# Kernel optimization log

Hardware: AMD Instinct MI355X
Metric: run time of the kernel (lower is better)

The kernel has to match this reference:

```python
import jax, jax.numpy as jnp
import numpy as np

# dims: G groups, A authors/group, P posts/author, DIN token-pooled feat, DEMB sentence-BERT dim
G, A, P, DIN, DEMB, HP, HA = 16, 64, 32, 768, 384, 256, 128


def setup_inputs() -> dict:
    key = jax.random.key(0)
    ks = jax.random.split(key, 8)
    s = lambda k, shape, scale: (jax.random.normal(k, shape, jnp.float32) * scale)
    return {
        "x": jax.random.normal(ks[0], (G, A, P, DIN), jnp.float32),
        "w_embed": s(ks[1], (DIN, DEMB), 0.02),   # BERT pooled-projection stand-in
        "b_embed": jnp.zeros((DEMB,), jnp.float32),
        "k_post": s(ks[2], (DEMB, 4 * HP), 0.05),  # Keras LSTM kernel, gates [i|f|c|o]
        "r_post": s(ks[3], (HP, 4 * HP), 0.05),    # recurrent kernel
        "b_post": jnp.zeros((4 * HP,), jnp.float32),
        "k_auth": s(ks[4], (HP, 4 * HA), 0.05),
        "r_auth": s(ks[5], (HA, 4 * HA), 0.05),
        "b_auth": jnp.zeros((4 * HA,), jnp.float32),
    }


def _lstm(x, Wk, Wr, b):
    """Keras-style LSTM, returns final hidden state. x: [B,T,D] -> [B,H]."""
    B = x.shape[0]
    H = Wr.shape[0]
    # precompute input projections for all timesteps in one GEMM: [T,B,4H]
    z = jnp.einsum('btd,dh->tbh', x, Wk) + b

    def step(carry, zt):
        h, c = carry
        g = zt + h @ Wr
        i, f, gg, o = jnp.split(g, 4, axis=-1)  # Keras gate order i,f,c,o
        c = jax.nn.sigmoid(f) * c + jax.nn.sigmoid(i) * jnp.tanh(gg)
        h = jax.nn.sigmoid(o) * jnp.tanh(c)
        return (h, c), None

    h0 = jnp.zeros((B, H), x.dtype)
    (h, _), _ = jax.lax.scan(step, (h0, h0), z)
    return h


def reference(x, w_embed, b_embed, k_post, r_post, b_post, k_auth, r_auth, b_auth):
    g, a, p, _ = x.shape
    # sentence embedding per post (BERT stand-in): [G,A,P,DEMB]
    e = jnp.einsum('gapd,de->gape', x, w_embed) + b_embed
    # LSTM over posts, batched across all (group, author) pairs: [G,A,HP]
    h_post = _lstm(e.reshape(g * a, p, e.shape[-1]), k_post, r_post, b_post)
    h_post = h_post.reshape(g, a, -1)
    # LSTM over authors: [G,HA]
    return _lstm(h_post, k_auth, r_auth, b_auth)
```

## Files before the change

### kernel.cpp

```cpp
#include <hip/hip_runtime.h>
#include <cstdint>
#include <cstddef>

#define G_    16
#define A_    64
#define P_    32
#define DIN_  768
#define DEMB_ 384
#define HP_   256
#define HA_   128
#define GA_   1024
#define N1_   1024
#define N2_   512
#define TCH   16

typedef float    f32x4   __attribute__((ext_vector_type(4)));
typedef _Float16 half8_t __attribute__((ext_vector_type(8)));
typedef _Float16 half4_t __attribute__((ext_vector_type(4)));

__device__ __forceinline__ float sigmoidf_(float x) { return 1.0f / (1.0f + __expf(-x)); }
__device__ __forceinline__ float tanhf_(float x) { return 2.0f / (1.0f + __expf(-2.0f * x)) - 1.0f; }
__device__ __forceinline__ _Float16 us2h(unsigned short u) { _Float16 h; __builtin_memcpy(&h, &u, 2); return h; }
__device__ __forceinline__ unsigned short h2us(_Float16 h) { unsigned short u; __builtin_memcpy(&u, &h, 2); return u; }


__global__ __launch_bounds__(256) void k_wk(const float* __restrict__ w_embed,
                                            const float* __restrict__ k_post,
                                            float* __restrict__ Bmat) {
    int j  = blockIdx.x * 256 + threadIdx.x;
    int k0 = blockIdx.y * 4;
    float acc0 = 0.f, acc1 = 0.f, acc2 = 0.f, acc3 = 0.f;
    for (int d = 0; d < DEMB_; ++d) {
        float kp = k_post[(size_t)d * N1_ + j];
        acc0 += w_embed[(size_t)(k0 + 0) * DEMB_ + d] * kp;
        acc1 += w_embed[(size_t)(k0 + 1) * DEMB_ + d] * kp;
        acc2 += w_embed[(size_t)(k0 + 2) * DEMB_ + d] * kp;
        acc3 += w_embed[(size_t)(k0 + 3) * DEMB_ + d] * kp;
    }
    Bmat[(size_t)(k0 + 0) * N1_ + j] = acc0;
    Bmat[(size_t)(k0 + 1) * N1_ + j] = acc1;
    Bmat[(size_t)(k0 + 2) * N1_ + j] = acc2;
    Bmat[(size_t)(k0 + 3) * N1_ + j] = acc3;
}

__global__ __launch_bounds__(256) void k_bias_p(const float* __restrict__ b_embed,
                                                const float* __restrict__ k_post,
                                                const float* __restrict__ b_post,
                                                float* __restrict__ biasZp) {
    int p = blockIdx.x * 256 + threadIdx.x;
    int n = (p >> 6) * 16 + (p & 15) + 256 * ((p >> 4) & 3);
    float acc = b_post[n];
    for (int d = 0; d < DEMB_; ++d)
        acc += b_embed[d] * k_post[(size_t)d * N1_ + n];
    biasZp[p] = acc;
}

__global__ __launch_bounds__(256) void k_t16(const float* __restrict__ Bmat,
                                             _Float16* __restrict__ Bt16) {
    __shared__ float tile[64][65];
    const int tid = threadIdx.x;
    const int p0 = blockIdx.x * 64;
    const int k0 = blockIdx.y * 64;
    const int jgrp = p0 >> 6;
#pragma unroll
    for (int i = 0; i < 16; ++i) {
        int idx = i * 256 + tid;
        int pp = idx & 63, kk = idx >> 6;
        int n = jgrp * 16 + (pp & 15) + 256 * ((pp >> 4) & 3);
        tile[pp][kk] = Bmat[(size_t)(k0 + kk) * N1_ + n];
    }
    __syncthreads();
    const int pp = tid >> 2;
    const int kq = (tid & 3) * 16;
    _Float16 buf[16];
#pragma unroll
    for (int i = 0; i < 16; ++i) buf[i] = (_Float16)tile[pp][kq + i];
    _Float16* dst = &Bt16[(size_t)(p0 + pp) * DIN_ + k0 + kq];
    *(half8_t*)dst       = *(half8_t*)&buf[0];
    *(half8_t*)(dst + 8) = *(half8_t*)&buf[8];
}

__global__ __launch_bounds__(256) void k_bfrag(const float* __restrict__ r_post,
                                               _Float16* __restrict__ Bfrag) {
    int idx = blockIdx.x * 256 + threadIdx.x;
    int pt = idx >> 9;
    int kt = (idx >> 6) & 7;
    int l  = idx & 63;
    int p = pt * 16 + (l & 15);
    int n = (p >> 6) * 16 + (p & 15) + 256 * ((p >> 4) & 3);
    int kb = kt * 32 + (l >> 4) * 8;
    _Float16 buf[8];
#pragma unroll
    for (int s = 0; s < 8; ++s) buf[s] = (_Float16)r_post[(size_t)(kb + s) * N1_ + n];
    *(half8_t*)&Bfrag[(size_t)idx * 8] = *(half8_t*)buf;
}

#define ZBM 128
#define ZBN 256
#define ZBK 32
#define ZPAD 40

struct ZgLDS {
    union {
        struct { _Float16 As[ZBM][ZPAD]; _Float16 Bs[ZBN][ZPAD]; } S;
        _Float16 Hs[64][264];
    } u;
};
struct RecLDS {
    _Float16 wlds[16 * 8 * 64 * 8];
    _Float16 hbuf[2][4096];
};

__device__ __forceinline__ void zgemm_core(ZgLDS* L, int bid, int tid,
                                           const float* __restrict__ x,
                                           const _Float16* __restrict__ Bt16,
                                           const float* __restrict__ biasZp,
                                           _Float16* __restrict__ Zq, int tbase) {
    const int wg = (bid & 7) * 64 + (bid >> 3);
    const int bm = (wg & 127) * ZBM;
    const int bn = (wg >> 7) * ZBN;

    const int arow = tid >> 3, akq = (tid & 7) * 4;
    const int brow = tid >> 2, bkq = (tid & 3) * 8;
    const int lane = tid & 63, w = tid >> 6;
    const int wm = (w >> 2) * 32, wn = (w & 3) * 64;
    const int frc = lane & 15, frk = (lane >> 4) * 8;

    const int crow = bm + arow;
    const size_t xrow = (size_t)(crow >> 4) * P_ + tbase + (crow & 15);
    const float*    aptr = &x[xrow * DIN_ + akq];
    const _Float16* bptr = &Bt16[(size_t)(bn + brow) * DIN_ + bkq];

    f32x4 acc[2][4];
#pragma unroll
    for (int i = 0; i < 2; ++i)
#pragma unroll
        for (int j = 0; j < 4; ++j) acc[i][j] = (f32x4)0.0f;

    float4 a0 = *(const float4*)aptr;
    uint4  b0 = *(const uint4*)bptr;

    const int NK = DIN_ / ZBK;
    for (int kt = 0; kt < NK; ++kt) {
        const int kn = (kt + 1 < NK) ? (kt + 1) * ZBK : kt * ZBK;
        float4 na0 = *(const float4*)(aptr + kn);
        uint4  nb0 = *(const uint4*)(bptr + kn);

        half4_t ahv;
        ahv[0] = (_Float16)a0.x; ahv[1] = (_Float16)a0.y;
        ahv[2] = (_Float16)a0.z; ahv[3] = (_Float16)a0.w;

        __syncthreads();
        *(half4_t*)&L->u.S.As[arow][akq] = ahv;
        *(uint4*)&L->u.S.Bs[brow][bkq]   = b0;
        __syncthreads();

        half8_t bf[4];
#pragma unroll
        for (int fn = 0; fn < 4; ++fn)
            bf[fn] = *(const half8_t*)&L->u.S.Bs[wn + fn * 16 + frc][frk];
#pragma unroll
        for (int fm = 0; fm < 2; ++fm) {
            half8_t aH = *(const half8_t*)&L->u.S.As[wm + fm * 16 + frc][frk];
#pragma unroll
            for (int fn = 0; fn < 4; ++fn)
                acc[fm][fn] = __builtin_amdgcn_mfma_f32_16x16x32_f16(aH, bf[fn], acc[fm][fn], 0, 0, 0);
        }
        a0 = na0; b0 = nb0;
    }

    float bzv[4];
#pragma unroll
    for (int fn = 0; fn < 4; ++fn) bzv[fn] = biasZp[bn + wn + fn * 16 + frc];

#pragma unroll
    for (int half_ = 0; half_ < 2; ++half_) {
        __syncthreads();
        if ((w >> 3) == half_) {
#pragma unroll
            for (int fm = 0; fm < 2; ++fm)
#pragma unroll
                for (int fn = 0; fn < 4; ++fn)
#pragma unroll
                    for (int r = 0; r < 4; ++r) {
                        int rl = ((w >> 2) & 1) * 32 + fm * 16 + (lane >> 4) * 4 + r;
                        int cl = wn + fn * 16 + frc;
                        int clp = ((cl >> 6) * 16 + (cl & 15)) * 4 + ((cl >> 4) & 3);
                        L->u.Hs[rl][clp] = (_Float16)(acc[fm][fn][r] + bzv[fn]);
                    }
        }
        __syncthreads();
        const int brb = (bm + half_ * 64) >> 4;
        const int rg  = brb >> 4;
        const int l4r = (brb & 15) >> 2;
        {
            int tloc = tid >> 6, hcl = tid & 63;
            _Float16 buf[16];
#pragma unroll
            for (int rr = 0; rr < 4; ++rr) {
                half4_t h4 = *(const half4_t*)&L->u.Hs[tloc + 16 * rr][hcl * 4];
                buf[rr * 4 + 0] = h4[0]; buf[rr * 4 + 1] = h4[1];
                buf[rr * 4 + 2] = h4[2]; buf[rr * 4 + 3] = h4[3];
            }
            int wvg  = (bn >> 6) + (hcl >> 4);
            int tid2 = wvg * 64 + l4r * 16 + (hcl & 15);
            _Float16* dst = &Zq[((size_t)(tloc * 64 + rg) * 1024 + tid2) * 16];
            *(uint4*)dst       = *(const uint4*)&buf[0];
            *(uint4*)(dst + 8) = *(const uint4*)&buf[8];
        }
    }
}

__device__ __forceinline__ void rec_core(RecLDS* L, int blk, int tid,
                                         const _Float16* __restrict__ Zq,
                                         const _Float16* __restrict__ Bfrag,
                                         float* __restrict__ csave,
                                         unsigned short* __restrict__ hsave,
                                         float* __restrict__ hF32, int tbase) {
    const int lane = tid & 63, wv = tid >> 6;
    const int hl = lane & 15, l4 = lane >> 4;
    const int r0 = blk * 16;
    const int hc = wv * 16 + hl;

    half8_t wreg[16];
#pragma unroll
    for (int q = 0; q < 2; ++q)
#pragma unroll
        for (int kt = 0; kt < 8; ++kt)
            wreg[q * 8 + kt] = *(const half8_t*)&Bfrag[(((size_t)(4 * wv + q) * 8 + kt) * 64 + lane) * 8];
#pragma unroll
    for (int kt = 0; kt < 8; ++kt)
        *(half8_t*)&L->wlds[((wv * 8 + kt) * 64 + lane) * 8] =
            *(const half8_t*)&Bfrag[(((size_t)(4 * wv + 2) * 8 + kt) * 64 + lane) * 8];
    const _Float16* w3base = &Bfrag[((size_t)(4 * wv + 3) * 8 * 64 + lane) * 8];

    float cst[4];
    if (tbase == 0) {
#pragma unroll
        for (int i = 0; i < 4; ++i) cst[i] = 0.f;
    } else {
        f32x4 cv = *(const f32x4*)&csave[((size_t)blk * 1024 + tid) * 4];
#pragma unroll
        for (int i = 0; i < 4; ++i) cst[i] = cv[i];
#pragma unroll
        for (int rr = 0; rr < 4; ++rr) {
            int row = l4 * 4 + rr;
            int lidx = (((hc >> 5) * 64) + (((hc & 31) >> 3) * 16 + row)) * 8 + (hc & 7);
            L->hbuf[0][lidx] = us2h(hsave[((size_t)(r0 + row)) * HP_ + hc]);
        }
    }
    __syncthreads();

    const _Float16* zp0 = &Zq[((size_t)blk * 1024 + tid) * 16];
    half8_t z01N = *(const half8_t*)zp0;
    half8_t z23N = *(const half8_t*)(zp0 + 8);

    for (int tt = 0; tt < TCH; ++tt) {
        const int t = tbase + tt;
        const int cur = t & 1, nxt = cur ^ 1;

        half8_t z01 = z01N, z23 = z23N;
        if (tt + 1 < TCH) {
            const _Float16* zpn = zp0 + (size_t)(tt + 1) * 1048576;
            z01N = *(const half8_t*)zpn;
            z23N = *(const half8_t*)(zpn + 8);
        }

        f32x4 acc[4];
#pragma unroll
        for (int i = 0; i < 4; ++i) acc[i] = (f32x4)0.0f;

        if (t > 0) {
#pragma unroll
            for (int kt = 0; kt < 8; ++kt) {
                half8_t ah = *(const half8_t*)&L->hbuf[cur][(kt * 64 + lane) * 8];
                half8_t b2 = *(const half8_t*)&L->wlds[((wv * 8 + kt) * 64 + lane) * 8];
                half8_t w3 = *(const half8_t*)&w3base[(size_t)kt * 512];
                acc[0] = __builtin_amdgcn_mfma_f32_16x16x32_f16(ah, wreg[kt],     acc[0], 0, 0, 0);
                acc[1] = __builtin_amdgcn_mfma_f32_16x16x32_f16(ah, wreg[8 + kt], acc[1], 0, 0, 0);
                acc[2] = __builtin_amdgcn_mfma_f32_16x16x32_f16(ah, b2,           acc[2], 0, 0, 0);
                acc[3] = __builtin_amdgcn_mfma_f32_16x16x32_f16(ah, w3,           acc[3], 0, 0, 0);
            }
        }

        const bool last = (t == P_ - 1);
        const bool save = (tbase == 0) && (tt == TCH - 1);
#pragma unroll
        for (int rr = 0; rr < 4; ++rr) {
            const half8_t zsrc = (rr < 2) ? z01 : z23;
            const int o = (rr & 1) * 4;
            float gi = acc[0][rr] + (float)zsrc[o + 0];
            float gf = acc[1][rr] + (float)zsrc[o + 1];
            float gg = acc[2][rr] + (float)zsrc[o + 2];
            float go = acc[3][rr] + (float)zsrc[o + 3];
            float cn = sigmoidf_(gf) * cst[rr] + sigmoidf_(gi) * tanhf_(gg);
            cst[rr] = cn;
            float hv = sigmoidf_(go) * tanhf_(cn);
            int row = l4 * 4 + rr;
            int lidx = (((hc >> 5) * 64) + (((hc & 31) >> 3) * 16 + row)) * 8 + (hc & 7);
            _Float16 hh = (_Float16)hv;
            L->hbuf[nxt][lidx] = hh;
            if (save) hsave[((size_t)(r0 + row)) * HP_ + hc] = h2us(hh);
            if (last) hF32[(size_t)(r0 + row) * HP_ + hc] = hv;
        }
        __syncthreads();
    }

    if (tbase == 0) {
        f32x4 cv;
#pragma unroll
        for (int i = 0; i < 4; ++i) cv[i] = cst[i];
        *(f32x4*)&csave[((size_t)blk * 1024 + tid) * 4] = cv;
    }
}

__global__ __launch_bounds__(1024, 4) void k_zgemm(const float* __restrict__ x,
                                                   const _Float16* __restrict__ Bt16,
                                                   const float* __restrict__ biasZp,
                                                   _Float16* __restrict__ Zq, int tbase) {
    __shared__ __align__(16) ZgLDS L;
    zgemm_core(&L, blockIdx.x, threadIdx.x, x, Bt16, biasZp, Zq, tbase);
}

__global__ __launch_bounds__(1024, 4) void k_rec(const _Float16* __restrict__ Zq,
                                                 const _Float16* __restrict__ Bfrag,
                                                 float* __restrict__ csave,
                                                 unsigned short* __restrict__ hsave,
                                                 float* __restrict__ hF32, int tbase) {
    __shared__ __align__(16) RecLDS L;
    rec_core(&L, blockIdx.x, threadIdx.x, Zq, Bfrag, csave, hsave, hF32, tbase);
}

__global__ __launch_bounds__(1024, 4) void k_fuse(const float* __restrict__ x,
                                                  const _Float16* __restrict__ Bt16,
                                                  const float* __restrict__ biasZp,
                                                  const _Float16* __restrict__ Zq0,
                                                  _Float16* __restrict__ Zq1,
                                                  const _Float16* __restrict__ Bfrag,
                                                  float* __restrict__ csave,
                                                  unsigned short* __restrict__ hsave,
                                                  float* __restrict__ hF32) {
    __shared__ __align__(16) union { RecLDS r; ZgLDS z; } L;
    if (blockIdx.x < 64)
        rec_core(&L.r, blockIdx.x, threadIdx.x, Zq0, Bfrag, csave, hsave, hF32, 0);
    else
        zgemm_core(&L.z, blockIdx.x - 64, threadIdx.x, x, Bt16, biasZp, Zq1, TCH);
}

__global__ __launch_bounds__(256) void k_zauth(const float* __restrict__ h,
                                               const float* __restrict__ k_auth,
                                               const float* __restrict__ b_auth,
                                               float* __restrict__ z_auth) {
    const int j = blockIdx.x * 256 + threadIdx.x;
    const int r0 = blockIdx.y * 4;
    float acc0 = b_auth[j], acc1 = acc0, acc2 = acc0, acc3 = acc0;
    for (int k = 0; k < HP_; ++k) {
        const float kp = k_auth[(size_t)k * N2_ + j];
        acc0 += h[(size_t)(r0 + 0) * HP_ + k] * kp;
        acc1 += h[(size_t)(r0 + 1) * HP_ + k] * kp;
        acc2 += h[(size_t)(r0 + 2) * HP_ + k] * kp;
        acc3 += h[(size_t)(r0 + 3) * HP_ + k] * kp;
    }
#pragma unroll
    for (int r = 0; r < 4; ++r) {
        const int b = r0 + r;
        const int g = b >> 6, a = b & 63;
        const float v = (r == 0) ? acc0 : (r == 1) ? acc1 : (r == 2) ? acc2 : acc3;
        z_auth[((size_t)a * G_ + g) * N2_ + j] = v;
    }
}

__global__ __launch_bounds__(1024) void k_author(const float* __restrict__ z_auth,
                                                 const float* __restrict__ r_auth,
                                                 float* __restrict__ out) {
    const int g = blockIdx.x;
    const int tid = threadIdx.x;
    const int j = tid & 511;
    const int kh = tid >> 9;

    __shared__ float hs[HA_];
    __shared__ float parts[2][512];

    float rc[64];
#pragma unroll
    for (int kk = 0; kk < 64; ++kk)
        rc[kk] = r_auth[(size_t)(kh * 64 + kk) * N2_ + j];

    float cj = 0.f;
    if (tid < HA_) hs[tid] = 0.f;
    __syncthreads();

    for (int a = 0; a < A_; ++a) {
        float acc = (kh == 0) ? z_auth[((size_t)a * G_ + g) * N2_ + j] : 0.f;
#pragma unroll
        for (int kk = 0; kk < 64; ++kk)
            acc += hs[kh * 64 + kk] * rc[kk];
        parts[kh][j] = acc;
        __syncthreads();
        if (tid < HA_) {
            float gi = parts[0][tid]       + parts[1][tid];
            float gf = parts[0][tid + 128] + parts[1][tid + 128];
            float gg = parts[0][tid + 256] + parts[1][tid + 256];
            float go = parts[0][tid + 384] + parts[1][tid + 384];
            cj = sigmoidf_(gf) * cj + sigmoidf_(gi) * tanhf_(gg);
            hs[tid] = sigmoidf_(go) * tanhf_(cj);
        }
        __syncthreads();
    }
    if (tid < HA_) out[(size_t)g * HA_ + tid] = hs[tid];
}

extern "C" void kernel_launch(void* const* d_in, const int* in_sizes, int n_in,
                              void* d_out, int out_size, void* d_ws, size_t ws_size,
                              hipStream_t stream) {
    const float* x       = (const float*)d_in[0];
    const float* w_embed = (const float*)d_in[1];
    const float* b_embed = (const float*)d_in[2];
    const float* k_post  = (const float*)d_in[3];
    const float* r_post  = (const float*)d_in[4];
    const float* b_post  = (const float*)d_in[5];
    const float* k_auth  = (const float*)d_in[6];
    const float* r_auth  = (const float*)d_in[7];
    const float* b_auth  = (const float*)d_in[8];
    float* out = (float*)d_out;

    char* wsb = (char*)d_ws;
    _Float16*       Zq0    = (_Float16*)(wsb);
    float*          Bmat   = (float*)(wsb + (32ull << 20));
    _Float16*       Bt16   = (_Float16*)(wsb + (36ull << 20));
    _Float16*       Bfrag  = (_Float16*)(wsb + (38ull << 20));
    float*          biasZp = (float*)(wsb + (38ull << 20) + (512ull << 10));
    float*          csave  = (float*)(wsb + (39ull << 20));
    unsigned short* hsave  = (unsigned short*)(wsb + (40ull << 20));
    float*          hF32   = (float*)(wsb + (41ull << 20));
    float*          z_auth = (float*)(wsb + (42ull << 20));
    _Float16*       Zq1    = (_Float16*)(wsb + (44ull << 20));

    const bool overlap = (ws_size >= (77ull << 20));

    k_wk    <<<dim3(N1_ / 256, DIN_ / 4), 256, 0, stream>>>(w_embed, k_post, Bmat);
    k_bias_p<<<dim3(N1_ / 256), 256, 0, stream>>>(b_embed, k_post, b_post, biasZp);
    k_t16   <<<dim3(16, 12), 256, 0, stream>>>(Bmat, Bt16);
    k_bfrag <<<dim3(128), 256, 0, stream>>>(r_post, Bfrag);

    k_zgemm<<<dim3(512), 1024, 0, stream>>>(x, Bt16, biasZp, Zq0, 0);

    if (overlap) {
        k_fuse<<<dim3(576), 1024, 0, stream>>>(x, Bt16, biasZp, Zq0, Zq1,
                                               Bfrag, csave, hsave, hF32);
        k_rec <<<dim3(64), 1024, 0, stream>>>(Zq1, Bfrag, csave, hsave, hF32, TCH);
    } else {
        k_rec  <<<dim3(64), 1024, 0, stream>>>(Zq0, Bfrag, csave, hsave, hF32, 0);
        k_zgemm<<<dim3(512), 1024, 0, stream>>>(x, Bt16, biasZp, Zq0, TCH);
        k_rec  <<<dim3(64), 1024, 0, stream>>>(Zq0, Bfrag, csave, hsave, hF32, TCH);
    }

    k_zauth <<<dim3(N2_ / 256, GA_ / 4), 256, 0, stream>>>(hF32, k_auth, b_auth, z_auth);
    k_author<<<dim3(G_), 1024, 0, stream>>>(z_auth, r_auth, out);
}
```

Baseline: 337.1 us.

## Pipeline input-projection GEMM and post LSTM per timestep via global flags

Replaces the two-chunk scheme (GEMM half, then fused rec+GEMM, then rec) with one persistent kernel. GEMM blocks each produce one timestep tile and bump a per-timestep atomic counter, and the 64 recurrence blocks spin on those counters before consuming each step. This removes the intermediate c/h save/restore and extra launches, and lets the recurrence start as soon as step 0 is ready. It relies on the recurrence blocks being co-resident with the GEMM blocks and on forward progress of the spin-waits; if scheduling orders blocks badly, this could deadlock or stall. The prefetch of the next step's Z is also removed.

```diff
diff --git a/kernel.cpp b/kernel.cpp
--- a/kernel.cpp
+++ b/kernel.cpp
@@ -111,14 +111,16 @@
     _Float16 hbuf[2][4096];
 };
 
-__device__ __forceinline__ void zgemm_core(ZgLDS* L, int bid, int tid,
-                                           const float* __restrict__ x,
-                                           const _Float16* __restrict__ Bt16,
-                                           const float* __restrict__ biasZp,
-                                           _Float16* __restrict__ Zq, int tbase) {
-    const int wg = (bid & 7) * 64 + (bid >> 3);
-    const int bm = (wg & 127) * ZBM;
-    const int bn = (wg >> 7) * ZBN;
+__device__ __forceinline__ void zg_t_core(ZgLDS* L, int b2, int tid,
+                                          const float* __restrict__ x,
+                                          const _Float16* __restrict__ Bt16,
+                                          const float* __restrict__ biasZp,
+                                          _Float16* __restrict__ Zq,
+                                          int* __restrict__ flags) {
+    const int t  = b2 >> 5;
+    const int tl = b2 & 31;
+    const int bm = (tl >> 2) * ZBM;
+    const int bn = (tl & 3) * ZBN;
 
     const int arow = tid >> 3, akq = (tid & 7) * 4;
     const int brow = tid >> 2, bkq = (tid & 3) * 8;
@@ -127,8 +129,7 @@
     const int frc = lane & 15, frk = (lane >> 4) * 8;
 
     const int crow = bm + arow;
-    const size_t xrow = (size_t)(crow >> 4) * P_ + tbase + (crow & 15);
-    const float*    aptr = &x[xrow * DIN_ + akq];
+    const float*    aptr = &x[((size_t)crow * P_ + t) * DIN_ + akq];
     const _Float16* bptr = &Bt16[(size_t)(bn + brow) * DIN_ + bkq];
 
     f32x4 acc[2][4];
@@ -190,33 +191,38 @@
                     }
         }
         __syncthreads();
-        const int brb = (bm + half_ * 64) >> 4;
-        const int rg  = brb >> 4;
-        const int l4r = (brb & 15) >> 2;
+        const int B0 = bm + half_ * 64;
         {
-            int tloc = tid >> 6, hcl = tid & 63;
+            int g4 = tid >> 6, hcl = tid & 63;
             _Float16 buf[16];
 #pragma unroll
             for (int rr = 0; rr < 4; ++rr) {
-                half4_t h4 = *(const half4_t*)&L->u.Hs[tloc + 16 * rr][hcl * 4];
+                half4_t h4 = *(const half4_t*)&L->u.Hs[g4 * 4 + rr][hcl * 4];
                 buf[rr * 4 + 0] = h4[0]; buf[rr * 4 + 1] = h4[1];
                 buf[rr * 4 + 2] = h4[2]; buf[rr * 4 + 3] = h4[3];
             }
+            int rg   = (B0 >> 4) + (g4 >> 2);
+            int l4r  = g4 & 3;
             int wvg  = (bn >> 6) + (hcl >> 4);
             int tid2 = wvg * 64 + l4r * 16 + (hcl & 15);
-            _Float16* dst = &Zq[((size_t)(tloc * 64 + rg) * 1024 + tid2) * 16];
+            _Float16* dst = &Zq[((size_t)(t * 64 + rg) * 1024 + tid2) * 16];
             *(uint4*)dst       = *(const uint4*)&buf[0];
             *(uint4*)(dst + 8) = *(const uint4*)&buf[8];
         }
     }
-}
-
-__device__ __forceinline__ void rec_core(RecLDS* L, int blk, int tid,
-                                         const _Float16* __restrict__ Zq,
-                                         const _Float16* __restrict__ Bfrag,
-                                         float* __restrict__ csave,
-                                         unsigned short* __restrict__ hsave,
-                                         float* __restrict__ hF32, int tbase) {
+
+    __syncthreads();
+    if (tid == 0) {
+        __threadfence();
+        __hip_atomic_fetch_add(&flags[t], 1, __ATOMIC_RELEASE, __HIP_MEMORY_SCOPE_AGENT);
+    }
+}
+
+__device__ __forceinline__ void rec32_core(RecLDS* L, int blk, int tid,
+                                           const _Float16* __restrict__ Zq,
+                                           const _Float16* __restrict__ Bfrag,
+                                           int* __restrict__ flags,
+                                           float* __restrict__ hF32) {
     const int lane = tid & 63, wv = tid >> 6;
     const int hl = lane & 15, l4 = lane >> 4;
     const int r0 = blk * 16;
@@ -234,37 +240,22 @@
             *(const half8_t*)&Bfrag[(((size_t)(4 * wv + 2) * 8 + kt) * 64 + lane) * 8];
     const _Float16* w3base = &Bfrag[((size_t)(4 * wv + 3) * 8 * 64 + lane) * 8];
 
-    float cst[4];
-    if (tbase == 0) {
-#pragma unroll
-        for (int i = 0; i < 4; ++i) cst[i] = 0.f;
-    } else {
-        f32x4 cv = *(const f32x4*)&csave[((size_t)blk * 1024 + tid) * 4];
-#pragma unroll
-        for (int i = 0; i < 4; ++i) cst[i] = cv[i];
-#pragma unroll
-        for (int rr = 0; rr < 4; ++rr) {
-            int row = l4 * 4 + rr;
-            int lidx = (((hc >> 5) * 64) + (((hc & 31) >> 3) * 16 + row)) * 8 + (hc & 7);
-            L->hbuf[0][lidx] = us2h(hsave[((size_t)(r0 + row)) * HP_ + hc]);
-        }
-    }
+    float cst[4] = {0.f, 0.f, 0.f, 0.f};
+    const _Float16* zp0 = &Zq[((size_t)blk * 1024 + tid) * 16];
     __syncthreads();
 
-    const _Float16* zp0 = &Zq[((size_t)blk * 1024 + tid) * 16];
-    half8_t z01N = *(const half8_t*)zp0;
-    half8_t z23N = *(const half8_t*)(zp0 + 8);
-
-    for (int tt = 0; tt < TCH; ++tt) {
-        const int t = tbase + tt;
+    for (int t = 0; t < P_; ++t) {
         const int cur = t & 1, nxt = cur ^ 1;
 
-        half8_t z01 = z01N, z23 = z23N;
-        if (tt + 1 < TCH) {
-            const _Float16* zpn = zp0 + (size_t)(tt + 1) * 1048576;
-            z01N = *(const half8_t*)zpn;
-            z23N = *(const half8_t*)(zpn + 8);
-        }
+        if (tid == 0) {
+            while (__hip_atomic_load(&flags[t], __ATOMIC_ACQUIRE, __HIP_MEMORY_SCOPE_AGENT) < 32)
+                __builtin_amdgcn_s_sleep(1);
+        }
+        __syncthreads();
+
+        const _Float16* zpt = zp0 + (size_t)t * 1048576;
+        half8_t z01 = *(const half8_t*)zpt;
+        half8_t z23 = *(const half8_t*)(zpt + 8);
 
         f32x4 acc[4];
 #pragma unroll
@@ -284,7 +275,6 @@
         }
 
         const bool last = (t == P_ - 1);
-        const bool save = (tbase == 0) && (tt == TCH - 1);
 #pragma unroll
         for (int rr = 0; rr < 4; ++rr) {
             const half8_t zsrc = (rr < 2) ? z01 : z23;
@@ -298,53 +288,42 @@
             float hv = sigmoidf_(go) * tanhf_(cn);
             int row = l4 * 4 + rr;
             int lidx = (((hc >> 5) * 64) + (((hc & 31) >> 3) * 16 + row)) * 8 + (hc & 7);
-            _Float16 hh = (_Float16)hv;
-            L->hbuf[nxt][lidx] = hh;
-            if (save) hsave[((size_t)(r0 + row)) * HP_ + hc] = h2us(hh);
+            L->hbuf[nxt][lidx] = (_Float16)hv;
             if (last) hF32[(size_t)(r0 + row) * HP_ + hc] = hv;
         }
         __syncthreads();
     }
-
-    if (tbase == 0) {
-        f32x4 cv;
-#pragma unroll
-        for (int i = 0; i < 4; ++i) cv[i] = cst[i];
-        *(f32x4*)&csave[((size_t)blk * 1024 + tid) * 4] = cv;
-    }
-}
-
-__global__ __launch_bounds__(1024, 4) void k_zgemm(const float* __restrict__ x,
-                                                   const _Float16* __restrict__ Bt16,
-                                                   const float* __restrict__ biasZp,
-                                                   _Float16* __restrict__ Zq, int tbase) {
-    __shared__ __align__(16) ZgLDS L;
-    zgemm_core(&L, blockIdx.x, threadIdx.x, x, Bt16, biasZp, Zq, tbase);
-}
-
-__global__ __launch_bounds__(1024, 4) void k_rec(const _Float16* __restrict__ Zq,
-                                                 const _Float16* __restrict__ Bfrag,
-                                                 float* __restrict__ csave,
-                                                 unsigned short* __restrict__ hsave,
-                                                 float* __restrict__ hF32, int tbase) {
-    __shared__ __align__(16) RecLDS L;
-    rec_core(&L, blockIdx.x, threadIdx.x, Zq, Bfrag, csave, hsave, hF32, tbase);
-}
-
-__global__ __launch_bounds__(1024, 4) void k_fuse(const float* __restrict__ x,
+}
+
+__global__ __launch_bounds__(1024, 4) void k_pipe(const float* __restrict__ x,
                                                   const _Float16* __restrict__ Bt16,
                                                   const float* __restrict__ biasZp,
-                                                  const _Float16* __restrict__ Zq0,
-                                                  _Float16* __restrict__ Zq1,
+                                                  _Float16* __restrict__ Zq,
                                                   const _Float16* __restrict__ Bfrag,
-                                                  float* __restrict__ csave,
-                                                  unsigned short* __restrict__ hsave,
+                                                  int* __restrict__ flags,
                                                   float* __restrict__ hF32) {
     __shared__ __align__(16) union { RecLDS r; ZgLDS z; } L;
     if (blockIdx.x < 64)
-        rec_core(&L.r, blockIdx.x, threadIdx.x, Zq0, Bfrag, csave, hsave, hF32, 0);
+        rec32_core(&L.r, blockIdx.x, threadIdx.x, Zq, Bfrag, flags, hF32);
     else
-        zgemm_core(&L.z, blockIdx.x - 64, threadIdx.x, x, Bt16, biasZp, Zq1, TCH);
+        zg_t_core(&L.z, blockIdx.x - 64, threadIdx.x, x, Bt16, biasZp, Zq, flags);
+}
+
+__global__ __launch_bounds__(1024, 4) void k_zgt(const float* __restrict__ x,
+                                                 const _Float16* __restrict__ Bt16,
+                                                 const float* __restrict__ biasZp,
+                                                 _Float16* __restrict__ Zq,
+                                                 int* __restrict__ flags) {
+    __shared__ __align__(16) ZgLDS L;
+    zg_t_core(&L, blockIdx.x, threadIdx.x, x, Bt16, biasZp, Zq, flags);
+}
+
+__global__ __launch_bounds__(1024, 4) void k_rec32(const _Float16* __restrict__ Zq,
+                                                   const _Float16* __restrict__ Bfrag,
+                                                   int* __restrict__ flags,
+                                                   float* __restrict__ hF32) {
+    __shared__ __align__(16) RecLDS L;
+    rec32_core(&L, blockIdx.x, threadIdx.x, Zq, Bfrag, flags, hF32);
 }
 
 __global__ __launch_bounds__(256) void k_zauth(const float* __restrict__ h,
@@ -425,34 +404,32 @@
     float* out = (float*)d_out;
 
     char* wsb = (char*)d_ws;
-    _Float16*       Zq0    = (_Float16*)(wsb);
-    float*          Bmat   = (float*)(wsb + (32ull << 20));
-    _Float16*       Bt16   = (_Float16*)(wsb + (36ull << 20));
-    _Float16*       Bfrag  = (_Float16*)(wsb + (38ull << 20));
-    float*          biasZp = (float*)(wsb + (38ull << 20) + (512ull << 10));
-    float*          csave  = (float*)(wsb + (39ull << 20));
-    unsigned short* hsave  = (unsigned short*)(wsb + (40ull << 20));
-    float*          hF32   = (float*)(wsb + (41ull << 20));
-    float*          z_auth = (float*)(wsb + (42ull << 20));
-    _Float16*       Zq1    = (_Float16*)(wsb + (44ull << 20));
-
-    const bool overlap = (ws_size >= (77ull << 20));
+    _Float16* Zq     = (_Float16*)(wsb);
+    float*    Bmat   = (float*)(wsb + (64ull << 20));
+    _Float16* Bt16   = (_Float16*)(wsb + (68ull << 20));
+    _Float16* Bfrag  = (_Float16*)(wsb + (70ull << 20));
+    float*    biasZp = (float*)(wsb + (70ull << 20) + (512ull << 10));
+    float*    hF32   = (float*)(wsb + (71ull << 20));
+    float*    z_auth = (float*)(wsb + (72ull << 20));
+    int*      flags  = (int*)(wsb + (74ull << 20));
+
+    const bool pipe = (ws_size >= (75ull << 20));
+    if (!pipe) {
+        Zq     = (_Float16*)(wsb);
+    }
+
+    hipMemsetAsync(flags, 0, 32 * sizeof(int), stream);
 
     k_wk    <<<dim3(N1_ / 256, DIN_ / 4), 256, 0, stream>>>(w_embed, k_post, Bmat);
     k_bias_p<<<dim3(N1_ / 256), 256, 0, stream>>>(b_embed, k_post, b_post, biasZp);
     k_t16   <<<dim3(16, 12), 256, 0, stream>>>(Bmat, Bt16);
     k_bfrag <<<dim3(128), 256, 0, stream>>>(r_post, Bfrag);
 
-    k_zgemm<<<dim3(512), 1024, 0, stream>>>(x, Bt16, biasZp, Zq0, 0);
-
-    if (overlap) {
-        k_fuse<<<dim3(576), 1024, 0, stream>>>(x, Bt16, biasZp, Zq0, Zq1,
-                                               Bfrag, csave, hsave, hF32);
-        k_rec <<<dim3(64), 1024, 0, stream>>>(Zq1, Bfrag, csave, hsave, hF32, TCH);
+    if (pipe) {
+        k_pipe<<<dim3(64 + 1024), 1024, 0, stream>>>(x, Bt16, biasZp, Zq, Bfrag, flags, hF32);
     } else {
-        k_rec  <<<dim3(64), 1024, 0, stream>>>(Zq0, Bfrag, csave, hsave, hF32, 0);
-        k_zgemm<<<dim3(512), 1024, 0, stream>>>(x, Bt16, biasZp, Zq0, TCH);
-        k_rec  <<<dim3(64), 1024, 0, stream>>>(Zq0, Bfrag, csave, hsave, hF32, TCH);
+        k_zgt  <<<dim3(1024), 1024, 0, stream>>>(x, Bt16, biasZp, Zq, flags);
+        k_rec32<<<dim3(64), 1024, 0, stream>>>(Zq, Bfrag, flags, hF32);
     }
 
     k_zauth <<<dim3(N2_ / 256, GA_ / 4), 256, 0, stream>>>(hF32, k_auth, b_auth, z_auth);
```

Result: slower. 461.0 us (+36.7%).
